# Kernel optimization log

Measured on AMD Instinct MI355X. Metric: run time of the kernel, lower is better.

The kernel has to match this reference:

```python
import jax, jax.numpy as jnp
import numpy as np
from functools import partial

B, S, I, H, L = 32, 512, 512, 512, 2  # batch, seq, input, hidden, layers (bidirectional)


def _uniform(key, shape, k):
    return jax.random.uniform(key, shape, jnp.float32, -k, k)


def setup_inputs() -> dict:
    key = jax.random.key(0)
    keys = jax.random.split(key, 1 + 16)
    inp = {"x": jax.random.normal(keys[0], (B, S, I), jnp.float32)}
    k = 1.0 / H
    ki = 1
    for l in range(L):
        in_sz = I if l == 0 else 2 * H
        for d in ("f", "b"):
            inp[f"w_ih_{l}{d}"] = _uniform(keys[ki], (4 * H, in_sz), k); ki += 1
            inp[f"w_hh_{l}{d}"] = _uniform(keys[ki], (4 * H, H), k); ki += 1
            inp[f"b_ih_{l}{d}"] = _uniform(keys[ki], (4 * H,), k); ki += 1
            inp[f"b_hh_{l}{d}"] = _uniform(keys[ki], (4 * H,), k); ki += 1
    return inp


def _lstm_dir(x_sbi, w_ih, w_hh, b_ih, b_hh, reverse):
    # x_sbi: [S,B,in]. Precompute input projection for all timesteps (one big GEMM).
    xp = jnp.einsum('sbi,gi->sbg', x_sbi, w_ih) + b_ih + b_hh  # [S,B,4H]
    h0 = jnp.zeros((x_sbi.shape[1], H), x_sbi.dtype)
    c0 = jnp.zeros_like(h0)

    def step(carry, xg):
        h, c = carry
        gates = xg + h @ w_hh.T
        i, f, g, o = jnp.split(gates, 4, axis=-1)  # pytorch order i,f,g,o
        i = jax.nn.sigmoid(i); f = jax.nn.sigmoid(f)
        g = jnp.tanh(g); o = jax.nn.sigmoid(o)
        c_new = f * c + i * g
        h_new = o * jnp.tanh(c_new)
        return (h_new, c_new), h_new

    (hT, cT), hs = jax.lax.scan(step, (h0, c0), xp, reverse=reverse)
    return hs, hT, cT  # hs in original time order [S,B,H]


def _forward(x, params):
    seq = jnp.transpose(x, (1, 0, 2))  # [S,B,I]
    final_h, final_c = [], []
    for l in range(L):
        hf, hTf, cTf = _lstm_dir(seq, *params[(l, 'f')], reverse=False)
        hb, hTb, cTb = _lstm_dir(seq, *params[(l, 'b')], reverse=True)
        seq = jnp.concatenate([hf, hb], axis=-1)  # [S,B,2H]
        final_h += [hTf, hTb]; final_c += [cTf, cTb]
    out = jnp.transpose(seq, (1, 0, 2))  # [B,S,2H]
    return out, (jnp.stack(final_h, 0), jnp.stack(final_c, 0))


def reference(x,
              w_ih_0f, w_hh_0f, b_ih_0f, b_hh_0f,
              w_ih_0b, w_hh_0b, b_ih_0b, b_hh_0b,
              w_ih_1f, w_hh_1f, b_ih_1f, b_hh_1f,
              w_ih_1b, w_hh_1b, b_ih_1b, b_hh_1b):
    params = {
        (0, 'f'): (w_ih_0f, w_hh_0f, b_ih_0f, b_hh_0f),
        (0, 'b'): (w_ih_0b, w_hh_0b, b_ih_0b, b_hh_0b),
        (1, 'f'): (w_ih_1f, w_hh_1f, b_ih_1f, b_hh_1f),
        (1, 'b'): (w_ih_1b, w_hh_1b, b_ih_1b, b_hh_1b),
    }
    return _forward(x, params)
```

## Files before the change

kernel.cpp:

```cpp
#include <hip/hip_runtime.h>

#define BB 32
#define SS 512
#define II 512
#define HH 512
#define GG 2048

typedef unsigned short u16;
typedef unsigned int   u32;
typedef unsigned long long u64;

typedef __attribute__((ext_vector_type(8))) short bf16x8;
typedef __attribute__((ext_vector_type(4))) float f32x4;

__device__ __forceinline__ float b2f(u16 h) {
    return __uint_as_float(((u32)h) << 16);
}
__device__ __forceinline__ u16 f2b(float f) {
    u32 u = __float_as_uint(f);
    u32 r = (u + 0x7FFFu + ((u >> 16) & 1u)) >> 16;
    return (u16)r;
}

#ifndef __has_builtin
#define __has_builtin(x) 0
#endif
#if __has_builtin(__builtin_amdgcn_global_load_lds)
#define HAVE_GLL 1
#else
#define HAVE_GLL 0
#endif

typedef __attribute__((address_space(1))) void as1_void;
typedef __attribute__((address_space(3))) void as3_void;

__device__ __forceinline__ void gload16(const void* g, void* l, int lane) {
#if HAVE_GLL
    __builtin_amdgcn_global_load_lds((as1_void*)g, (as3_void*)l, 16, 0, 0);
#else
    *(bf16x8*)((char*)l + lane * 16) = *(const bf16x8*)g;
#endif
}

__global__ void k_convert_x(const float* __restrict__ x, u16* __restrict__ xbf) {
    const int n4 = BB * SS * II / 4;
    for (int e4 = blockIdx.x * blockDim.x + threadIdx.x; e4 < n4;
         e4 += gridDim.x * blockDim.x) {
        int e = e4 * 4;
        int s = e >> 14;
        int b = (e >> 9) & 31;
        int i = e & 511;
        float4 v = *(const float4*)(x + (size_t)b * (SS * II) + (size_t)s * II + i);
        ushort4 o;
        o.x = f2b(v.x); o.y = f2b(v.y); o.z = f2b(v.z); o.w = f2b(v.w);
        *(ushort4*)(xbf + (size_t)s * (BB * II) + (size_t)b * II + i) = o;
    }
}

__global__ void k_cast(const float* __restrict__ src, u16* __restrict__ dst, int n4) {
    for (int e4 = blockIdx.x * blockDim.x + threadIdx.x; e4 < n4;
         e4 += gridDim.x * blockDim.x) {
        float4 v = *(const float4*)(src + (size_t)e4 * 4);
        ushort4 o;
        o.x = f2b(v.x); o.y = f2b(v.y); o.z = f2b(v.z); o.w = f2b(v.w);
        *(ushort4*)(dst + (size_t)e4 * 4) = o;
    }
}

#define BKP 64

__launch_bounds__(256)
__global__ void k_proj(const u16* __restrict__ A,
                       const u16* __restrict__ Wf_, const u16* __restrict__ Wb_,
                       const float* __restrict__ bihf, const float* __restrict__ bhhf,
                       const float* __restrict__ bihb, const float* __restrict__ bhhb,
                       u16* __restrict__ xpf, u16* __restrict__ xpb,
                       int K) {
    const int dir = blockIdx.z;
    const u16* Wm = dir ? Wb_ : Wf_;
    const float* bih = dir ? bihb : bihf;
    const float* bhh = dir ? bhhb : bhhf;
    u16* xp = dir ? xpb : xpf;

    __shared__ __align__(16) u16 As[128 * BKP];
    __shared__ __align__(16) u16 Bs[128 * BKP];

    const int t    = threadIdx.x;
    const int lane = t & 63;
    const int w    = t >> 6;
    const int wm   = w >> 1, wn = w & 1;
    const int m0   = blockIdx.x * 128;
    const int n0   = blockIdx.y * 128;

    f32x4 acc[4][4] = {};

    for (int kt = 0; kt < K; kt += BKP) {
        #pragma unroll
        for (int i = 0; i < 4; ++i) {
            int c   = (w * 4 + i) * 64 + lane;
            int row = c >> 3;
            int lc  = (c & 7) ^ (row & 7);
            int gk  = kt + lc * 8;
            gload16(A  + (size_t)(m0 + row) * K + gk, (char*)As + (w * 4 + i) * 1024, lane);
            gload16(Wm + (size_t)(n0 + row) * K + gk, (char*)Bs + (w * 4 + i) * 1024, lane);
        }
        __syncthreads();

        #pragma unroll
        for (int ks = 0; ks < 2; ++ks) {
            const int kc = ks * 4 + (lane >> 4);
            bf16x8 af[4], bfr[4];
            #pragma unroll
            for (int mi = 0; mi < 4; ++mi) {
                int row = wm * 64 + mi * 16 + (lane & 15);
                af[mi] = *(const bf16x8*)&As[row * BKP + ((kc ^ (row & 7)) << 3)];
            }
            #pragma unroll
            for (int ni = 0; ni < 4; ++ni) {
                int row = wn * 64 + ni * 16 + (lane & 15);
                bfr[ni] = *(const bf16x8*)&Bs[row * BKP + ((kc ^ (row & 7)) << 3)];
            }
            #pragma unroll
            for (int mi = 0; mi < 4; ++mi)
                #pragma unroll
                for (int ni = 0; ni < 4; ++ni)
                    acc[mi][ni] = __builtin_amdgcn_mfma_f32_16x16x32_bf16(
                        af[mi], bfr[ni], acc[mi][ni], 0, 0, 0);
        }
        __syncthreads();
    }

    #pragma unroll
    for (int ni = 0; ni < 4; ++ni) {
        int n = n0 + wn * 64 + ni * 16 + (lane & 15);
        float bias = bih[n] + bhh[n];
        #pragma unroll
        for (int mi = 0; mi < 4; ++mi) {
            #pragma unroll
            for (int r = 0; r < 4; ++r) {
                int m = m0 + wm * 64 + mi * 16 + (lane >> 4) * 4 + r;
                xp[(size_t)m * GG + n] = f2b(acc[mi][ni][r] + bias);
            }
        }
    }
}

__launch_bounds__(512, 1)
__global__ void k_rec(const u16* __restrict__ xpf, const u16* __restrict__ xpb,
                      const float* __restrict__ whf, const float* __restrict__ whb,
                      u64* __restrict__ Hd,
                      u16* __restrict__ hs0,
                      float* __restrict__ out,
                      float* __restrict__ fin,
                      int layer) {
    const int bid  = blockIdx.x;
    const int dir  = bid >> 5;
    const int wg   = bid & 31;
    const int j0   = wg * 16;
    const u16*  xp = dir ? xpb : xpf;
    const float* W = dir ? whb : whf;

    const int t    = threadIdx.x;
    const int lane = t & 63;
    const int wv   = t >> 6;
    const int g    = wv & 3;
    const int m    = wv >> 2;

    __shared__ __align__(16) u16 Wfr[64 * 64 * 8];
    __shared__ __align__(16) u16 hl[32 * 512];
    __shared__ float xq[2][32 * 65];
    __shared__ float gates[4 * 32 * 18];

    for (int it = 0; it < 8; ++it) {
        int task = it * 512 + t;
        int l    = task & 63;
        int blk  = task >> 6;
        int gg   = blk >> 4;
        int kt   = blk & 15;
        const float* src = W + (size_t)(gg * 512 + j0 + (l & 15)) * 512
                             + kt * 32 + (l >> 4) * 8;
        float4 v0 = *(const float4*)src;
        float4 v1 = *(const float4*)(src + 4);
        union { bf16x8 v; u16 a[8]; } u;
        u.a[0] = f2b(v0.x); u.a[1] = f2b(v0.y); u.a[2] = f2b(v0.z); u.a[3] = f2b(v0.w);
        u.a[4] = f2b(v1.x); u.a[5] = f2b(v1.y); u.a[6] = f2b(v1.z); u.a[7] = f2b(v1.w);
        *(bf16x8*)&Wfr[task * 8] = u.v;
    }
    __syncthreads();

    const int wd   = t & 255;
    const int r0   = (t >> 8) * 16;
    const int sc_c   = wd >> 2;
    const int sc_sub = (wd & 3) * 4;

    const int eb = t >> 4;
    const int ej = t & 15;
    float creg = 0.f;

    u64 w[16];

    for (int s = 0; s < SS; ++s) {
        const int sa = dir ? (SS - 1 - s) : s;

        if (t < 256) {
            int b = t & 31, seg = t >> 5;
            int gq = seg >> 1, hf = seg & 1;
            const u16* xsrc = xp + (size_t)(sa * 32 + b) * GG + gq * 512 + j0 + hf * 8;
            bf16x8 v0 = *(const bf16x8*)xsrc;
            float* xdst = &xq[s & 1][b * 65 + gq * 16 + hf * 8];
            #pragma unroll
            for (int i = 0; i < 8; ++i) xdst[i] = b2f((u16)v0[i]);
        }

        if (s > 0) {
            const u64* Hrd = Hd + ((size_t)((s & 1) * 2 + dir)) * (32 * 256);
            const u32 tgt = (u32)((layer << 10) | s);
            for (;;) {
                bool ok = true;
                #pragma unroll
                for (int i = 0; i < 16; ++i) {
                    ok = ok && (((u32)w[i] & 0xffffu) == tgt)
                            && ((((u32)(w[i] >> 32)) & 0xffffu) == tgt);
                }
                if (ok) break;
                #pragma unroll
                for (int i = 0; i < 16; ++i)
                    w[i] = __hip_atomic_load(Hrd + (r0 + i) * 256 + wd,
                                             __ATOMIC_RELAXED, __HIP_MEMORY_SCOPE_AGENT);
            }
            #pragma unroll
            for (int i = 0; i < 16; ++i) {
                int r = r0 + i;
                u32 two = (u32)((w[i] >> 16) & 0xffffu) | ((u32)(w[i] >> 48) << 16);
                int off = r * 1024 + ((sc_c ^ (r & 7)) << 4) + sc_sub;
                *(u32*)((char*)hl + off) = two;
            }
        } else {
            #pragma unroll
            for (int i = 0; i < 16; ++i) {
                int r = r0 + i;
                int off = r * 1024 + ((sc_c ^ (r & 7)) << 4) + sc_sub;
                *(u32*)((char*)hl + off) = 0u;
            }
        }
        __syncthreads();

        {
            f32x4 acc = {0.f, 0.f, 0.f, 0.f};
            const int b0 = lane & 15, q = lane >> 4;
            #pragma unroll
            for (int kt = 0; kt < 16; ++kt) {
                int pc = ((kt << 2) + q) ^ (b0 & 7);
                bf16x8 a0 = *(const bf16x8*)&hl[(b0 + m * 16) * 512 + pc * 8];
                bf16x8 Bv = *(const bf16x8*)&Wfr[((g * 16 + kt) * 64 + lane) * 8];
                acc = __builtin_amdgcn_mfma_f32_16x16x32_bf16(a0, Bv, acc, 0, 0, 0);
            }
            #pragma unroll
            for (int r = 0; r < 4; ++r)
                gates[g * 576 + (m * 16 + q * 4 + r) * 18 + b0] = acc[r];
        }
        __syncthreads();

        {
            const float* xrow = &xq[s & 1][eb * 65];
            float gi = xrow[     ej] + gates[0 * 576 + eb * 18 + ej];
            float gf = xrow[16 + ej] + gates[1 * 576 + eb * 18 + ej];
            float gg = xrow[32 + ej] + gates[2 * 576 + eb * 18 + ej];
            float go = xrow[48 + ej] + gates[3 * 576 + eb * 18 + ej];
            float ig = 1.f / (1.f + __expf(-gi));
            float fg = 1.f / (1.f + __expf(-gf));
            float gt = tanhf(gg);
            float og = 1.f / (1.f + __expf(-go));
            float c  = fg * creg + ig * gt;
            float h  = og * tanhf(c);
            creg = c;

            u32* Hwr32 = (u32*)(Hd + ((size_t)(((s + 1) & 1) * 2 + dir)) * (32 * 256));
            const u32 pst = (u32)((layer << 10) | (s + 1));
            __hip_atomic_store(Hwr32 + eb * 512 + j0 + ej,
                               ((u32)f2b(h) << 16) | pst,
                               __ATOMIC_RELAXED, __HIP_MEMORY_SCOPE_AGENT);

            if (s + 1 < SS) {
                const u64* Hn = Hd + ((size_t)(((s + 1) & 1) * 2 + dir)) * (32 * 256);
                #pragma unroll
                for (int i = 0; i < 16; ++i)
                    w[i] = __hip_atomic_load(Hn + (r0 + i) * 256 + wd,
                                             __ATOMIC_RELAXED, __HIP_MEMORY_SCOPE_AGENT);
            }

            if (layer == 0) {
                hs0[(size_t)sa * (BB * 1024) + (size_t)eb * 1024 + dir * 512 + j0 + ej]
                    = f2b(h);
            } else {
                out[(size_t)eb * (SS * 1024) + (size_t)sa * 1024 + dir * 512 + j0 + ej] = h;
            }
            if (s == SS - 1) {
                int sl = layer * 2 + dir;
                fin[(size_t)sl * (32 * 512) + eb * 512 + j0 + ej] = h;
                fin[65536 + (size_t)sl * (32 * 512) + eb * 512 + j0 + ej] = c;
            }
        }
    }
}

#define OFF_XBF   ((size_t)0)
#define OFF_HS0   ((size_t)16777216)
#define OFF_XPF   ((size_t)50331648)
#define OFF_XPB   ((size_t)117440512)
#define OFF_WIH0F ((size_t)184549376)
#define OFF_WIH0B ((size_t)186646528)
#define OFF_WIH1F ((size_t)188743680)
#define OFF_WIH1B ((size_t)192937984)
#define OFF_HST   ((size_t)197132288)

extern "C" void kernel_launch(void* const* d_in, const int* in_sizes, int n_in,
                              void* d_out, int out_size, void* d_ws, size_t ws_size,
                              hipStream_t stream) {
    const float* x      = (const float*)d_in[0];
    const float* wih0f  = (const float*)d_in[1];
    const float* whh0f  = (const float*)d_in[2];
    const float* bih0f  = (const float*)d_in[3];
    const float* bhh0f  = (const float*)d_in[4];
    const float* wih0b  = (const float*)d_in[5];
    const float* whh0b  = (const float*)d_in[6];
    const float* bih0b  = (const float*)d_in[7];
    const float* bhh0b  = (const float*)d_in[8];
    const float* wih1f  = (const float*)d_in[9];
    const float* whh1f  = (const float*)d_in[10];
    const float* bih1f  = (const float*)d_in[11];
    const float* bhh1f  = (const float*)d_in[12];
    const float* wih1b  = (const float*)d_in[13];
    const float* whh1b  = (const float*)d_in[14];
    const float* bih1b  = (const float*)d_in[15];
    const float* bhh1b  = (const float*)d_in[16];

    float* out = (float*)d_out;
    char* ws = (char*)d_ws;

    u16* xbf    = (u16*)(ws + OFF_XBF);
    u16* hs0    = (u16*)(ws + OFF_HS0);
    u16* xpf    = (u16*)(ws + OFF_XPF);
    u16* xpb    = (u16*)(ws + OFF_XPB);
    u16* bwih0f = (u16*)(ws + OFF_WIH0F);
    u16* bwih0b = (u16*)(ws + OFF_WIH0B);
    u16* bwih1f = (u16*)(ws + OFF_WIH1F);
    u16* bwih1b = (u16*)(ws + OFF_WIH1B);
    u64* Hd     = (u64*)(ws + OFF_HST);
    float* fin  = out + 16777216;

    k_convert_x<<<1024, 256, 0, stream>>>(x, xbf);
    k_cast<<<512, 256, 0, stream>>>(wih0f, bwih0f, 2048 * 512 / 4);
    k_cast<<<512, 256, 0, stream>>>(wih0b, bwih0b, 2048 * 512 / 4);
    k_cast<<<512, 256, 0, stream>>>(wih1f, bwih1f, 2048 * 1024 / 4);
    k_cast<<<512, 256, 0, stream>>>(wih1b, bwih1b, 2048 * 1024 / 4);

    hipMemsetAsync(ws + OFF_HST, 0, 262144, stream);

    k_proj<<<dim3(128, 16, 2), 256, 0, stream>>>(
        xbf, bwih0f, bwih0b, bih0f, bhh0f, bih0b, bhh0b, xpf, xpb, 512);
    k_rec<<<64, 512, 0, stream>>>(xpf, xpb, whh0f, whh0b, Hd,
                                  hs0, nullptr, fin, 0);

    k_proj<<<dim3(128, 16, 2), 256, 0, stream>>>(
        hs0, bwih1f, bwih1b, bih1f, bhh1f, bih1b, bhh1b, xpf, xpb, 1024);
    k_rec<<<64, 512, 0, stream>>>(xpf, xpb, whh1f, whh1b, Hd,
                                  nullptr, out, fin, 1);
}
```

Before: 5.741 ms.

## Interleave gate columns per wave to drop block barrier after MFMA

```diff
diff --git a/kernel.cpp b/kernel.cpp
--- a/kernel.cpp
+++ b/kernel.cpp
@@ -163,58 +163,66 @@
     const int t    = threadIdx.x;
     const int lane = t & 63;
     const int wv   = t >> 6;
-    const int g    = wv & 3;
+    const int cg   = wv & 3;
     const int m    = wv >> 2;
 
-    __shared__ __align__(16) u16 Wfr[64 * 64 * 8];
+    __shared__ __align__(16) u16 Wfr[4][16][512];
     __shared__ __align__(16) u16 hl[32 * 512];
-    __shared__ float xq[2][32 * 65];
-    __shared__ float gates[4 * 32 * 18];
+    __shared__ float xq[2][32 * 68];
+    __shared__ float scr[8][320];
 
     for (int it = 0; it < 8; ++it) {
         int task = it * 512 + t;
         int l    = task & 63;
         int blk  = task >> 6;
-        int gg   = blk >> 4;
+        int pcg  = blk >> 4;
         int kt   = blk & 15;
-        const float* src = W + (size_t)(gg * 512 + j0 + (l & 15)) * 512
-                             + kt * 32 + (l >> 4) * 8;
+        int r    = l & 15;
+        int grow = (r >> 2) * 512 + j0 + pcg * 4 + (r & 3);
+        const float* src = W + (size_t)grow * 512 + kt * 32 + (l >> 4) * 8;
         float4 v0 = *(const float4*)src;
         float4 v1 = *(const float4*)(src + 4);
         union { bf16x8 v; u16 a[8]; } u;
         u.a[0] = f2b(v0.x); u.a[1] = f2b(v0.y); u.a[2] = f2b(v0.z); u.a[3] = f2b(v0.w);
         u.a[4] = f2b(v1.x); u.a[5] = f2b(v1.y); u.a[6] = f2b(v1.z); u.a[7] = f2b(v1.w);
-        *(bf16x8*)&Wfr[task * 8] = u.v;
+        *(bf16x8*)&Wfr[pcg][kt][l * 8] = u.v;
     }
     __syncthreads();
 
-    const int wd   = t & 255;
-    const int r0   = (t >> 8) * 16;
+    const int wd     = t & 255;
+    const int r0     = (t >> 8) * 16;
     const int sc_c   = wd >> 2;
     const int sc_sub = (wd & 3) * 4;
 
-    const int eb = t >> 4;
-    const int ej = t & 15;
+    const int bl   = lane >> 2;
+    const int cc   = lane & 3;
+    const int eb   = m * 16 + bl;
+    const int ecol = j0 + cg * 4 + cc;
     float creg = 0.f;
-
-    u64 w[16];
 
     for (int s = 0; s < SS; ++s) {
         const int sa = dir ? (SS - 1 - s) : s;
 
-        if (t < 256) {
-            int b = t & 31, seg = t >> 5;
-            int gq = seg >> 1, hf = seg & 1;
-            const u16* xsrc = xp + (size_t)(sa * 32 + b) * GG + gq * 512 + j0 + hf * 8;
-            bf16x8 v0 = *(const bf16x8*)xsrc;
-            float* xdst = &xq[s & 1][b * 65 + gq * 16 + hf * 8];
-            #pragma unroll
-            for (int i = 0; i < 8; ++i) xdst[i] = b2f((u16)v0[i]);
-        }
-
+        u64 w[16];
+        const u64* Hrd = Hd + ((size_t)((s & 1) * 2 + dir)) * (32 * 256);
+        const u32 tgt = (u32)((layer << 10) | s);
         if (s > 0) {
-            const u64* Hrd = Hd + ((size_t)((s & 1) * 2 + dir)) * (32 * 256);
-            const u32 tgt = (u32)((layer << 10) | s);
+            #pragma unroll
+            for (int i = 0; i < 16; ++i)
+                w[i] = __hip_atomic_load(Hrd + (r0 + i) * 256 + wd,
+                                         __ATOMIC_RELAXED, __HIP_MEMORY_SCOPE_AGENT);
+        }
+
+        {
+            int b = t >> 4, seg = t & 15;
+            int g = seg >> 2, j4 = (seg & 3) * 4;
+            const u16* xsrc = xp + (size_t)(sa * 32 + b) * GG + g * 512 + j0 + j4;
+            ushort4 v = *(const ushort4*)xsrc;
+            float* xd = &xq[s & 1][b * 68 + g * 16 + j4];
+            xd[0] = b2f(v.x); xd[1] = b2f(v.y); xd[2] = b2f(v.z); xd[3] = b2f(v.w);
+        }
+
+        if (s > 0) {
             for (;;) {
                 bool ok = true;
                 #pragma unroll
@@ -222,7 +230,7 @@
                     ok = ok && (((u32)w[i] & 0xffffu) == tgt)
                             && ((((u32)(w[i] >> 32)) & 0xffffu) == tgt);
                 }
-                if (ok) break;
+                if (__all(ok)) break;
                 #pragma unroll
                 for (int i = 0; i < 16; ++i)
                     w[i] = __hip_atomic_load(Hrd + (r0 + i) * 256 + wd,
@@ -245,28 +253,30 @@
         }
         __syncthreads();
 
+        f32x4 acc = {0.f, 0.f, 0.f, 0.f};
         {
-            f32x4 acc = {0.f, 0.f, 0.f, 0.f};
             const int b0 = lane & 15, q = lane >> 4;
             #pragma unroll
             for (int kt = 0; kt < 16; ++kt) {
                 int pc = ((kt << 2) + q) ^ (b0 & 7);
                 bf16x8 a0 = *(const bf16x8*)&hl[(b0 + m * 16) * 512 + pc * 8];
-                bf16x8 Bv = *(const bf16x8*)&Wfr[((g * 16 + kt) * 64 + lane) * 8];
+                bf16x8 Bv = *(const bf16x8*)&Wfr[cg][kt][lane * 8];
                 acc = __builtin_amdgcn_mfma_f32_16x16x32_bf16(a0, Bv, acc, 0, 0, 0);
             }
-            #pragma unroll
-            for (int r = 0; r < 4; ++r)
-                gates[g * 576 + (m * 16 + q * 4 + r) * 18 + b0] = acc[r];
-        }
-        __syncthreads();
+            const int r = lane & 15;
+            #pragma unroll
+            for (int reg = 0; reg < 4; ++reg)
+                scr[wv][(q * 4 + reg) * 20 + (r & 3) * 4 + (r >> 2)] = acc[reg];
+        }
+        asm volatile("s_waitcnt lgkmcnt(0)" ::: "memory");
+        __builtin_amdgcn_sched_barrier(0);
 
         {
-            const float* xrow = &xq[s & 1][eb * 65];
-            float gi = xrow[     ej] + gates[0 * 576 + eb * 18 + ej];
-            float gf = xrow[16 + ej] + gates[1 * 576 + eb * 18 + ej];
-            float gg = xrow[32 + ej] + gates[2 * 576 + eb * 18 + ej];
-            float go = xrow[48 + ej] + gates[3 * 576 + eb * 18 + ej];
+            const float* xrow = &xq[s & 1][eb * 68];
+            float gi = scr[wv][bl * 20 + cc * 4 + 0] + xrow[0 * 16 + cg * 4 + cc];
+            float gf = scr[wv][bl * 20 + cc * 4 + 1] + xrow[1 * 16 + cg * 4 + cc];
+            float gg = scr[wv][bl * 20 + cc * 4 + 2] + xrow[2 * 16 + cg * 4 + cc];
+            float go = scr[wv][bl * 20 + cc * 4 + 3] + xrow[3 * 16 + cg * 4 + cc];
             float ig = 1.f / (1.f + __expf(-gi));
             float fg = 1.f / (1.f + __expf(-gf));
             float gt = tanhf(gg);
@@ -277,28 +287,20 @@
 
             u32* Hwr32 = (u32*)(Hd + ((size_t)(((s + 1) & 1) * 2 + dir)) * (32 * 256));
             const u32 pst = (u32)((layer << 10) | (s + 1));
-            __hip_atomic_store(Hwr32 + eb * 512 + j0 + ej,
+            __hip_atomic_store(Hwr32 + eb * 512 + ecol,
                                ((u32)f2b(h) << 16) | pst,
                                __ATOMIC_RELAXED, __HIP_MEMORY_SCOPE_AGENT);
 
-            if (s + 1 < SS) {
-                const u64* Hn = Hd + ((size_t)(((s + 1) & 1) * 2 + dir)) * (32 * 256);
-                #pragma unroll
-                for (int i = 0; i < 16; ++i)
-                    w[i] = __hip_atomic_load(Hn + (r0 + i) * 256 + wd,
-                                             __ATOMIC_RELAXED, __HIP_MEMORY_SCOPE_AGENT);
-            }
-
             if (layer == 0) {
-                hs0[(size_t)sa * (BB * 1024) + (size_t)eb * 1024 + dir * 512 + j0 + ej]
+                hs0[(size_t)sa * (BB * 1024) + (size_t)eb * 1024 + dir * 512 + ecol]
                     = f2b(h);
             } else {
-                out[(size_t)eb * (SS * 1024) + (size_t)sa * 1024 + dir * 512 + j0 + ej] = h;
+                out[(size_t)eb * (SS * 1024) + (size_t)sa * 1024 + dir * 512 + ecol] = h;
             }
             if (s == SS - 1) {
                 int sl = layer * 2 + dir;
-                fin[(size_t)sl * (32 * 512) + eb * 512 + j0 + ej] = h;
-                fin[65536 + (size_t)sl * (32 * 512) + eb * 512 + j0 + ej] = c;
+                fin[(size_t)sl * (32 * 512) + eb * 512 + ecol] = h;
+                fin[65536 + (size_t)sl * (32 * 512) + eb * 512 + ecol] = c;
             }
         }
     }
```

After: 5.775 ms. No clear change (+0.6%).
